# Performance work log

Measured on AMD Instinct MI355X. Metric: run time of the kernel, lower is better.

## Reference

```python
import jax, jax.numpy as jnp
import numpy as np

HEAD = 64            # RWKV_HEAD_SIZE
C = 1024             # n_embd = dim_att
F = 4096             # dim_ffn
B, T = 8, 256
H = C // HEAD
N_LAYER, LAYER_ID = 12, 1
GN_EPS = 1e-5 * 8 ** 2   # GroupNorm eps = 1e-5 * head_size_divisor^2


def bshift(x):
    """bidirectional_shift_multihead: per head, first half of channels shifted
    forward in time (right), second half shifted backward (left), zero-padded."""
    b, t, c = x.shape
    x4 = x.reshape(b, t, c // HEAD, HEAD)
    mid = HEAD // 2
    f = jnp.pad(x4[:, :-1, :, :mid], ((0, 0), (1, 0), (0, 0), (0, 0)))
    r = jnp.pad(x4[:, 1:, :, mid:], ((0, 0), (0, 1), (0, 0), (0, 0)))
    return jnp.concatenate([f, r], -1).reshape(b, t, c)


def layernorm(x, g, b):
    m = jnp.mean(x, -1, keepdims=True)
    v = jnp.mean((x - m) ** 2, -1, keepdims=True)
    return (x - m) * jax.lax.rsqrt(v + 1e-5) * g + b


def groupnorm(x, g, b):
    bb, t, c = x.shape
    xg = x.reshape(bb, t, H, HEAD)
    m = jnp.mean(xg, -1, keepdims=True)
    v = jnp.mean((xg - m) ** 2, -1, keepdims=True)
    return ((xg - m) * jax.lax.rsqrt(v + GN_EPS)).reshape(bb, t, c) * g + b


def wkv6_bi(r, k, v, w, u):
    """Bidirectional WKV6. r,k,v,w: [B,T,H,N]; u: [H,N].
    y_t = r_t . (S^fwd_t + u*k_t v_t^T + S^bwd_t), with per-channel decay
    d_t = exp(-exp(w_t)) applied to the state after each step in each direction."""
    d = jnp.exp(-jnp.exp(w))
    rT, kT, vT, dT = (jnp.moveaxis(a, 1, 0) for a in (r, k, v, d))  # [T,B,H,N]
    S0 = jnp.zeros((B, H, HEAD, HEAD), r.dtype)
    uB = u[None]  # [1,H,N]

    def fstep(S, inp):
        rt, kt, vt, dt = inp
        kv = kt[..., None] * vt[..., None, :]              # [B,H,N,N]
        y = jnp.einsum('bhj,bhji->bhi', rt, S + uB[..., None] * kv)
        return dt[..., None] * S + kv, y

    _, yf = jax.lax.scan(fstep, S0, (rT, kT, vT, dT))

    def bstep(S, inp):
        rt, kt, vt, dt = inp
        y = jnp.einsum('bhj,bhji->bhi', rt, S)
        return dt[..., None] * S + kt[..., None] * vt[..., None, :], y

    _, yb = jax.lax.scan(bstep, S0, (rT, kT, vT, dT), reverse=True)
    return jnp.moveaxis(yf + yb, 0, 1)  # [B,T,H,N]


def block_forward(x, ln1_g, ln1_b, ln2_g, ln2_b,
                  maa_x, maa_w, maa_k, maa_v, maa_r, maa_g, maa_w1, maa_w2,
                  time_decay, tdw1, tdw2, u, Wr, Wk, Wv, Wg, Wo, lnx_g, lnx_b,
                  cmaa_k, cmaa_r, Wck, Wcv, Wcr):
    # ---- RWKV_Tmix_V6 (attention) branch ----
    xa = layernorm(x, ln1_g, ln1_b)
    xx = bshift(xa) - xa
    a = jnp.tanh((xa + xx * maa_x) @ maa_w1).reshape(B, T, 5, -1)   # [B,T,5,32]
    m = jnp.einsum('btfd,fdc->fbtc', a, maa_w2)                      # [5,B,T,C]
    xw = xa + xx * (maa_w + m[0])
    xk = xa + xx * (maa_k + m[1])
    xv = xa + xx * (maa_v + m[2])
    xr = xa + xx * (maa_r + m[3])
    xg = xa + xx * (maa_g + m[4])
    r = (xr @ Wr).reshape(B, T, H, HEAD)
    k = (xk @ Wk).reshape(B, T, H, HEAD)
    v = (xv @ Wv).reshape(B, T, H, HEAD)
    g = jax.nn.silu(xg @ Wg)
    w = (time_decay + jnp.tanh(xw @ tdw1) @ tdw2).reshape(B, T, H, HEAD)
    y = wkv6_bi(r, k, v, w, u).reshape(B, T, C)
    y = groupnorm(y, lnx_g, lnx_b)
    x = x + (y * g) @ Wo
    # ---- RWKV_CMix_V6 (FFN) branch ----
    xc = layernorm(x, ln2_g, ln2_b)
    cxx = bshift(xc) - xc
    kk = jnp.square(jax.nn.relu((xc + cxx * cmaa_k) @ Wck))
    kv = kk @ Wcv
    x = x + jax.nn.sigmoid((xc + cxx * cmaa_r) @ Wcr) * kv
    return x


def setup_inputs() -> dict:
    key = jax.random.key(0)
    ks = jax.random.split(key, 16)
    r1 = 1.0 - LAYER_ID / N_LAYER            # ratio_1_to_almost0
    r0 = LAYER_ID / (N_LAYER - 1)            # ratio_0_to_1
    ddd = np.arange(C, dtype=np.float64) / C
    base = (1.0 - ddd ** r1).astype(np.float32)
    half = (1.0 - ddd ** (0.5 * r1)).astype(np.float32)
    s = 0.02
    p = {}
    p['x'] = jax.random.normal(ks[0], (B, T, C), jnp.float32)
    p['ln1_g'] = jnp.ones((C,), jnp.float32)
    p['ln1_b'] = jnp.zeros((C,), jnp.float32)
    p['ln2_g'] = jnp.ones((C,), jnp.float32)
    p['ln2_b'] = jnp.zeros((C,), jnp.float32)
    p['maa_x'] = jnp.asarray(base)
    p['maa_w'] = jnp.asarray(base)
    p['maa_k'] = jnp.asarray(base)
    p['maa_v'] = jnp.asarray((1.0 - (ddd ** r1 + 0.3 * r0)).astype(np.float32))
    p['maa_r'] = jnp.asarray(half)
    p['maa_g'] = jnp.asarray(half)
    p['maa_w1'] = jax.random.uniform(ks[1], (C, 160), jnp.float32, -0.01, 0.01)
    p['maa_w2'] = jax.random.uniform(ks[2], (5, 32, C), jnp.float32, -0.01, 0.01)
    n = np.arange(C, dtype=np.float64)
    p['time_decay'] = jnp.asarray((-6.0 + 5.0 * (n / (C - 1)) ** (0.7 + 1.3 * r0)).astype(np.float32))
    p['tdw1'] = jax.random.uniform(ks[3], (C, 64), jnp.float32, -0.01, 0.01)
    p['tdw2'] = jax.random.uniform(ks[4], (64, C), jnp.float32, -0.01, 0.01)
    faaaa = r0 * (1.0 - n / (C - 1)) + ((n + 1) % 3 - 1) * 0.1
    p['u'] = jnp.asarray(faaaa.reshape(H, HEAD).astype(np.float32))
    p['Wr'] = jax.random.normal(ks[5], (C, C), jnp.float32) * s
    p['Wk'] = jax.random.normal(ks[6], (C, C), jnp.float32) * s
    p['Wv'] = jax.random.normal(ks[7], (C, C), jnp.float32) * s
    p['Wg'] = jax.random.normal(ks[8], (C, C), jnp.float32) * s
    p['Wo'] = jax.random.normal(ks[9], (C, C), jnp.float32) * s
    p['lnx_g'] = jnp.ones((C,), jnp.float32)
    p['lnx_b'] = jnp.zeros((C,), jnp.float32)
    p['cmaa_k'] = jnp.asarray(base)
    p['cmaa_r'] = jnp.asarray(base)
    p['Wck'] = jax.random.normal(ks[10], (C, F), jnp.float32) * s
    p['Wcv'] = jax.random.normal(ks[11], (F, C), jnp.float32) * s
    p['Wcr'] = jax.random.normal(ks[12], (C, C), jnp.float32) * s
    return p


def reference(x, ln1_g, ln1_b, ln2_g, ln2_b,
              maa_x, maa_w, maa_k, maa_v, maa_r, maa_g, maa_w1, maa_w2,
              time_decay, tdw1, tdw2, u, Wr, Wk, Wv, Wg, Wo, lnx_g, lnx_b,
              cmaa_k, cmaa_r, Wck, Wcv, Wcr):
    return block_forward(x, ln1_g, ln1_b, ln2_g, ln2_b,
                         maa_x, maa_w, maa_k, maa_v, maa_r, maa_g, maa_w1, maa_w2,
                         time_decay, tdw1, tdw2, u, Wr, Wk, Wv, Wg, Wo, lnx_g, lnx_b,
                         cmaa_k, cmaa_r, Wck, Wcv, Wcr)
```

## Files before the change

### kernel.cpp

```cpp
#include <hip/hip_runtime.h>
#include <math.h>
#include <stdint.h>

static constexpr int B  = 8;
static constexpr int T  = 256;
static constexpr int C  = 1024;
static constexpr int H  = 16;
static constexpr int HEAD = 64;
static constexpr int FF = 4096;
static constexpr int BT = B * T;
static constexpr int NCH = 8;
static constexpr int CS  = 32;

typedef short short8  __attribute__((ext_vector_type(8)));
typedef float floatx4 __attribute__((ext_vector_type(4)));

__device__ __forceinline__ float bf2f(ushort u) {
    return __uint_as_float(((uint32_t)u) << 16);
}
__device__ __forceinline__ ushort f2bf(float x) {
    uint32_t u = __float_as_uint(x);
    u += 0x7fff + ((u >> 16) & 1);
    return (ushort)(u >> 16);
}

__device__ __forceinline__ void gload16(const void* g, void* l) {
    __builtin_amdgcn_global_load_lds(
        (const __attribute__((address_space(1))) unsigned int*)g,
        (__attribute__((address_space(3))) unsigned int*)l, 16, 0, 0);
}

#define BEPI_NONE_BF   0
#define BEPI_SILU_BF   1
#define BEPI_RELUSQ_BF 2
#define BEPI_NONE_F    3
#define BEPI_RES_F     4
#define BEPI_SIGRES_F  5
#define BEPI_TANH_F    6
#define BEPI_TANH_BF   7
#define BEPI_DECAY_F   8
#define BEPI_SIGRES2_F 9

__device__ __forceinline__ void red6(float (&vals)[6], float* red)
{
    const int wave = threadIdx.x >> 6, lane = threadIdx.x & 63;
#pragma unroll
    for (int i = 0; i < 6; ++i) {
        float v = vals[i];
#pragma unroll
        for (int off = 32; off > 0; off >>= 1) v += __shfl_xor(v, off);
        if (lane == 0) red[i * 4 + wave] = v;
    }
    __syncthreads();
#pragma unroll
    for (int i = 0; i < 6; ++i)
        vals[i] = red[i * 4 + 0] + red[i * 4 + 1] + red[i * 4 + 2] + red[i * 4 + 3];
}

__global__ __launch_bounds__(256) void lnshiftmix_kernel(const float* __restrict__ x,
                                                         const float* __restrict__ g,
                                                         const float* __restrict__ b,
                                                         const float* __restrict__ maa,
                                                         float* __restrict__ xa,
                                                         float* __restrict__ xx,
                                                         ushort* __restrict__ ax)
{
    const int row = blockIdx.x;
    const int t = row & (T - 1);
    const int tid = threadIdx.x;
    __shared__ float red[24];
    const float4 vc = reinterpret_cast<const float4*>(x + (size_t)row * C)[tid];
    float4 vp = make_float4(0.f, 0.f, 0.f, 0.f), vn = make_float4(0.f, 0.f, 0.f, 0.f);
    if (t > 0)     vp = reinterpret_cast<const float4*>(x + (size_t)(row - 1) * C)[tid];
    if (t < T - 1) vn = reinterpret_cast<const float4*>(x + (size_t)(row + 1) * C)[tid];
    float vals[6];
    vals[0] = vc.x + vc.y + vc.z + vc.w;
    vals[1] = vc.x * vc.x + vc.y * vc.y + vc.z * vc.z + vc.w * vc.w;
    vals[2] = vp.x + vp.y + vp.z + vp.w;
    vals[3] = vp.x * vp.x + vp.y * vp.y + vp.z * vp.z + vp.w * vp.w;
    vals[4] = vn.x + vn.y + vn.z + vn.w;
    vals[5] = vn.x * vn.x + vn.y * vn.y + vn.z * vn.z + vn.w * vn.w;
    red6(vals, red);
    const float mc = vals[0] * (1.f / C);
    const float rc = rsqrtf(fmaxf(vals[1] * (1.f / C) - mc * mc, 0.f) + 1e-5f);
    const float mp = vals[2] * (1.f / C);
    const float rp = rsqrtf(fmaxf(vals[3] * (1.f / C) - mp * mp, 0.f) + 1e-5f);
    const float mn = vals[4] * (1.f / C);
    const float rn = rsqrtf(fmaxf(vals[5] * (1.f / C) - mn * mn, 0.f) + 1e-5f);

    const int c = tid * 4;
    const bool fh = ((c & 63) < 32);
    const float cur[4] = {vc.x, vc.y, vc.z, vc.w};
    const float nbr[4] = {fh ? vp.x : vn.x, fh ? vp.y : vn.y,
                          fh ? vp.z : vn.z, fh ? vp.w : vn.w};
    const float mN = fh ? mp : mn, rN = fh ? rp : rn;
    const bool nvalid = fh ? (t > 0) : (t < T - 1);
    const size_t rb = (size_t)row * C;
#pragma unroll
    for (int e = 0; e < 4; ++e) {
        const float gg = g[c + e], bb = b[c + e];
        const float av = (cur[e] - mc) * rc * gg + bb;
        const float sv = nvalid ? ((nbr[e] - mN) * rN * gg + bb) : 0.f;
        const float xv = sv - av;
        xa[rb + c + e] = av;
        xx[rb + c + e] = xv;
        ax[rb + c + e] = f2bf(av + xv * maa[c + e]);
    }
}

__global__ __launch_bounds__(256) void lnshiftcmix_kernel(const float* __restrict__ x,
                                                          const float* __restrict__ g,
                                                          const float* __restrict__ b,
                                                          const float* __restrict__ mk,
                                                          const float* __restrict__ mr,
                                                          ushort* __restrict__ ok,
                                                          ushort* __restrict__ orr)
{
    const int row = blockIdx.x;
    const int t = row & (T - 1);
    const int tid = threadIdx.x;
    __shared__ float red[24];
    const float4 vc = reinterpret_cast<const float4*>(x + (size_t)row * C)[tid];
    float4 vp = make_float4(0.f, 0.f, 0.f, 0.f), vn = make_float4(0.f, 0.f, 0.f, 0.f);
    if (t > 0)     vp = reinterpret_cast<const float4*>(x + (size_t)(row - 1) * C)[tid];
    if (t < T - 1) vn = reinterpret_cast<const float4*>(x + (size_t)(row + 1) * C)[tid];
    float vals[6];
    vals[0] = vc.x + vc.y + vc.z + vc.w;
    vals[1] = vc.x * vc.x + vc.y * vc.y + vc.z * vc.z + vc.w * vc.w;
    vals[2] = vp.x + vp.y + vp.z + vp.w;
    vals[3] = vp.x * vp.x + vp.y * vp.y + vp.z * vp.z + vp.w * vp.w;
    vals[4] = vn.x + vn.y + vn.z + vn.w;
    vals[5] = vn.x * vn.x + vn.y * vn.y + vn.z * vn.z + vn.w * vn.w;
    red6(vals, red);
    const float mc = vals[0] * (1.f / C);
    const float rc = rsqrtf(fmaxf(vals[1] * (1.f / C) - mc * mc, 0.f) + 1e-5f);
    const float mp = vals[2] * (1.f / C);
    const float rp = rsqrtf(fmaxf(vals[3] * (1.f / C) - mp * mp, 0.f) + 1e-5f);
    const float mn = vals[4] * (1.f / C);
    const float rn = rsqrtf(fmaxf(vals[5] * (1.f / C) - mn * mn, 0.f) + 1e-5f);

    const int c = tid * 4;
    const bool fh = ((c & 63) < 32);
    const float cur[4] = {vc.x, vc.y, vc.z, vc.w};
    const float nbr[4] = {fh ? vp.x : vn.x, fh ? vp.y : vn.y,
                          fh ? vp.z : vn.z, fh ? vp.w : vn.w};
    const float mN = fh ? mp : mn, rN = fh ? rp : rn;
    const bool nvalid = fh ? (t > 0) : (t < T - 1);
    const size_t rb = (size_t)row * C;
#pragma unroll
    for (int e = 0; e < 4; ++e) {
        const float gg = g[c + e], bb = b[c + e];
        const float av = (cur[e] - mc) * rc * gg + bb;
        const float sv = nvalid ? ((nbr[e] - mN) * rN * gg + bb) : 0.f;
        const float xv = sv - av;
        ok[rb + c + e]  = f2bf(av + xv * mk[c + e]);
        orr[rb + c + e] = f2bf(av + xv * mr[c + e]);
    }
}

__global__ __launch_bounds__(1024) void gnmul_kernel(const ushort* __restrict__ yf,
                                                     const ushort* __restrict__ yb,
                                                     const float* __restrict__ g,
                                                     const float* __restrict__ b,
                                                     const ushort* __restrict__ gate,
                                                     const ushort* __restrict__ vin,
                                                     const ushort* __restrict__ rbuf,
                                                     const ushort* __restrict__ kbuf,
                                                     const float* __restrict__ u,
                                                     ushort* __restrict__ out)
{
    const int row = blockIdx.x;
    const int tid = threadIdx.x;
    const size_t idx = (size_t)row * C + tid;
    float p = bf2f(rbuf[idx]) * bf2f(kbuf[idx]) * u[tid];
#pragma unroll
    for (int off = 32; off > 0; off >>= 1) p += __shfl_xor(p, off);
    const float v = bf2f(yf[idx]) + bf2f(yb[idx]) + p * bf2f(vin[idx]);
    float s = v;
#pragma unroll
    for (int off = 32; off > 0; off >>= 1) s += __shfl_xor(s, off);
    const float m = s * (1.0f / HEAD);
    const float d = v - m;
    float q = d * d;
#pragma unroll
    for (int off = 32; off > 0; off >>= 1) q += __shfl_xor(q, off);
    const float rstd = rsqrtf(q * (1.0f / HEAD) + 6.4e-4f);
    out[idx] = f2bf((d * rstd * g[tid] + b[tid]) * bf2f(gate[idx]));
}

__global__ __launch_bounds__(256) void wconv_kernel(const float* __restrict__ W,
                                                    ushort* __restrict__ Wt,
                                                    int Kd, int Nd)
{
    __shared__ float tile[32][33];
    const int n0 = blockIdx.x * 32, k0 = blockIdx.y * 32;
    const int tx = threadIdx.x, ty = threadIdx.y;
#pragma unroll
    for (int i = 0; i < 4; ++i)
        tile[ty * 4 + i][tx] = W[(size_t)(k0 + ty * 4 + i) * Nd + n0 + tx];
    __syncthreads();
#pragma unroll
    for (int i = 0; i < 4; ++i)
        Wt[(size_t)(n0 + ty * 4 + i) * Kd + k0 + tx] = f2bf(tile[tx][ty * 4 + i]);
}

__global__ __launch_bounds__(256) void w2conv_kernel(const float* __restrict__ w2,
                                                     ushort* __restrict__ w2t)
{
    __shared__ float tile[32][33];
    const int f = blockIdx.y;
    const int n0 = blockIdx.x * 32;
    const int tx = threadIdx.x, ty = threadIdx.y;
#pragma unroll
    for (int i = 0; i < 4; ++i)
        tile[ty * 4 + i][tx] = w2[(size_t)f * 32 * C + (size_t)(ty * 4 + i) * C + n0 + tx];
    __syncthreads();
#pragma unroll
    for (int i = 0; i < 4; ++i)
        w2t[(size_t)f * C * 32 + (size_t)(n0 + ty * 4 + i) * 32 + tx] = f2bf(tile[tx][ty * 4 + i]);
}

struct Wconv4Args { const float* W[4]; };
__global__ __launch_bounds__(256) void wconv4_kernel(Wconv4Args args, ushort* __restrict__ Wt)
{
    __shared__ float tile[32][33];
    const int z = blockIdx.z;
    const float* __restrict__ W = args.W[z];
    ushort* __restrict__ dst = Wt + (size_t)z * C * C;
    const int n0 = blockIdx.x * 32, k0 = blockIdx.y * 32;
    const int tx = threadIdx.x, ty = threadIdx.y;
#pragma unroll
    for (int i = 0; i < 4; ++i)
        tile[ty * 4 + i][tx] = W[(size_t)(k0 + ty * 4 + i) * C + n0 + tx];
    __syncthreads();
#pragma unroll
    for (int i = 0; i < 4; ++i)
        dst[(size_t)(n0 + ty * 4 + i) * C + k0 + tx] = f2bf(tile[tx][ty * 4 + i]);
}

struct Mix5Args { const float* maa[5]; ushort* out[5]; };
__global__ __launch_bounds__(256) void mix5m_kernel(const ushort* __restrict__ a5b,
                                                    const ushort* __restrict__ w2t,
                                                    const float* __restrict__ xa,
                                                    const float* __restrict__ xx,
                                                    Mix5Args args)
{
    __shared__ __align__(16) ushort As[128 * 32];
    __shared__ __align__(16) ushort Bs[64 * 32];
    const int f = blockIdx.z;
    const int bm = blockIdx.y * 128, bn = blockIdx.x * 64;
    const int tid = threadIdx.x;
    const int wid = tid >> 6, lane = tid & 63;
    const int wr = wid >> 1, wc = wid & 1;
    const int l15 = lane & 15, lhi = lane >> 4;

#pragma unroll
    for (int p = 0; p < 2; ++p) {
        const int lin = p * 256 + tid;
        const int row = lin >> 2;
        const int sp = (lin & 3) ^ ((row >> 1) & 3);
        gload16(a5b + (size_t)(bm + row) * 160 + f * 32 + sp * 8, &As[lin * 8]);
    }
    {
        const int lin = tid;
        const int n = lin >> 2;
        const int sp = (lin & 3) ^ ((n >> 1) & 3);
        gload16(w2t + ((size_t)f * C + bn + n) * 32 + sp * 8, &Bs[lin * 8]);
    }
    __syncthreads();

    short8 af[4], bfr[2];
#pragma unroll
    for (int m = 0; m < 4; ++m) {
        const int row = wr * 64 + m * 16 + l15;
        const int sp = lhi ^ ((row >> 1) & 3);
        af[m] = *(const short8*)&As[row * 32 + sp * 8];
    }
#pragma unroll
    for (int n = 0; n < 2; ++n) {
        const int col = wc * 32 + n * 16 + l15;
        const int sp = lhi ^ ((col >> 1) & 3);
        bfr[n] = *(const short8*)&Bs[col * 32 + sp * 8];
    }
    floatx4 acc[4][2];
#pragma unroll
    for (int m = 0; m < 4; ++m)
#pragma unroll
        for (int n = 0; n < 2; ++n)
            acc[m][n] = __builtin_amdgcn_mfma_f32_16x16x32_bf16(
                af[m], bfr[n], (floatx4){0.f, 0.f, 0.f, 0.f}, 0, 0, 0);

    const float* __restrict__ maa = args.maa[f];
    ushort* __restrict__ out = args.out[f];
#pragma unroll
    for (int m = 0; m < 4; ++m) {
        const int row0 = bm + wr * 64 + m * 16 + lhi * 4;
#pragma unroll
        for (int n = 0; n < 2; ++n) {
            const int col = bn + wc * 32 + n * 16 + l15;
            const float mc = maa[col];
#pragma unroll
            for (int j = 0; j < 4; ++j) {
                const size_t oi = (size_t)(row0 + j) * C + col;
                out[oi] = f2bf(xa[oi] + xx[oi] * (mc + acc[m][n][j]));
            }
        }
    }
}

__global__ __launch_bounds__(256) void wkv_pass1(const ushort* __restrict__ k,
                                                 const ushort* __restrict__ v,
                                                 const float* __restrict__ d,
                                                 ushort* __restrict__ M,
                                                 float* __restrict__ D)
{
    const int uc = blockIdx.x;
    const int c = uc & (NCH - 1), unit = uc >> 3;
    const int dir = unit & 1, bh = unit >> 1;
    const int tid = threadIdx.x;
    const int wv = tid >> 6, lane = tid & 63;
    const int l15 = lane & 15, lhi = lane >> 4;
    const size_t rowb = ((size_t)(bh >> 4) * T * H + (bh & 15)) * HEAD;
    const int s0 = c * CS;

    __shared__ ushort kT[64][40];
    __shared__ ushort vt[64][40];
    __shared__ float  Ldd[CS][64];

    for (int idx = tid; idx < CS * 64; idx += 256) {
        const int s = idx >> 6, j = idx & 63;
        const int t = dir ? (T - 1 - (s0 + s)) : (s0 + s);
        const size_t g = rowb + (size_t)t * (H * HEAD) + j;
        kT[j][s] = k[g];
        vt[j][s] = v[g];
        Ldd[s][j] = d[g];
    }
    __syncthreads();

    if (tid < 64) {
        const int j = tid;
        float G = 1.f;
#pragma unroll
        for (int s = CS - 1; s >= 0; --s) {
            kT[j][s] = f2bf(bf2f(kT[j][s]) * G);
            G *= Ldd[s][j];
        }
        D[(size_t)uc * 64 + j] = G;
    }
    __syncthreads();

    const short8 av = *(const short8*)&vt[wv * 16 + l15][lhi * 8];
    ushort* __restrict__ mrow = M + (size_t)uc * 4096;
#pragma unroll
    for (int n = 0; n < 4; ++n) {
        const short8 bk = *(const short8*)&kT[n * 16 + l15][lhi * 8];
        const floatx4 acc = __builtin_amdgcn_mfma_f32_16x16x32_bf16(
            av, bk, (floatx4){0.f, 0.f, 0.f, 0.f}, 0, 0, 0);
#pragma unroll
        for (int jr = 0; jr < 4; ++jr) {
            const int i = wv * 16 + lhi * 4 + jr;
            mrow[(size_t)i * 64 + n * 16 + l15] = f2bf(acc[jr]);
        }
    }
}

__global__ __launch_bounds__(1024) void wkv_pass2(ushort* __restrict__ M,
                                                  const float* __restrict__ D)
{
    const int unit = blockIdx.x;
    const int tid = threadIdx.x;
    const int j0 = (tid & 15) * 4;
    float S0 = 0.f, S1 = 0.f, S2 = 0.f, S3 = 0.f;
#pragma unroll
    for (int c = 0; c < NCH; ++c) {
        const int uc = unit * NCH + c;
        const float4 Dv = *reinterpret_cast<const float4*>(D + (size_t)uc * 64 + j0);
        ushort* mp = M + (size_t)uc * 4096 + tid * 4;
        const uint2 mv = *reinterpret_cast<const uint2*>(mp);
        const float m0 = bf2f((ushort)(mv.x & 0xffff));
        const float m1 = bf2f((ushort)(mv.x >> 16));
        const float m2 = bf2f((ushort)(mv.y & 0xffff));
        const float m3 = bf2f((ushort)(mv.y >> 16));
        uint2 sv;
        sv.x = (uint32_t)f2bf(S0) | ((uint32_t)f2bf(S1) << 16);
        sv.y = (uint32_t)f2bf(S2) | ((uint32_t)f2bf(S3) << 16);
        *reinterpret_cast<uint2*>(mp) = sv;
        S0 = fmaf(Dv.x, S0, m0);
        S1 = fmaf(Dv.y, S1, m1);
        S2 = fmaf(Dv.z, S2, m2);
        S3 = fmaf(Dv.w, S3, m3);
    }
}

__global__ __launch_bounds__(256) void wkv_ymfma(const ushort* __restrict__ r,
                                                 const ushort* __restrict__ k,
                                                 const ushort* __restrict__ v,
                                                 const float* __restrict__ d,
                                                 const ushort* __restrict__ Sin,
                                                 ushort* __restrict__ yf,
                                                 ushort* __restrict__ yb)
{
    const int uc = blockIdx.x;
    const int c = uc & (NCH - 1), unit = uc >> 3;
    const int dir = unit & 1, bh = unit >> 1;
    const int tid = threadIdx.x;
    const int wv = tid >> 6, lane = tid & 63;
    const int l15 = lane & 15, lhi = lane >> 4;
    const size_t rowb = ((size_t)(bh >> 4) * T * H + (bh & 15)) * HEAD;
    const int s0 = c * CS;

    __shared__ ushort rp[32][64];
    __shared__ ushort kp[32][64];
    __shared__ ushort vt[64][40];
    __shared__ ushort Pl[32][32];
    __shared__ float  Ldd[CS][64];

    for (int idx = tid; idx < 32 * 64; idx += 256) {
        const int s = idx >> 6, j = idx & 63;
        const int t = dir ? (T - 1 - (s0 + s)) : (s0 + s);
        const size_t g = rowb + (size_t)t * (H * HEAD) + j;
        const int cs = (j >> 3) ^ (s & 7);
        rp[s][cs * 8 + (j & 7)] = r[g];
        kp[s][cs * 8 + (j & 7)] = k[g];
        vt[j][s] = v[g];
        Ldd[s][j] = d[g];
    }
    __syncthreads();

    if (wv == 0) {
        const int j = lane;
        float Q = 1.f;
#pragma unroll
        for (int s = 0; s < 32; ++s) {
            const int a = ((j >> 3) ^ (s & 7)) * 8 + (j & 7);
            rp[s][a] = f2bf(bf2f(rp[s][a]) * Q);
            Q *= Ldd[s][j];
        }
    } else if (wv == 1) {
        const int j = lane;
        float iQ = 1.f;
#pragma unroll
        for (int s = 0; s < 32; ++s) {
            iQ *= (1.0f / Ldd[s][j]);
            const int a = ((j >> 3) ^ (s & 7)) * 8 + (j & 7);
            kp[s][a] = f2bf(bf2f(kp[s][a]) * iQ);
        }
    }
    __syncthreads();

    const int st = wv & 1;
    const int ip = wv >> 1;

    short8 ar[2];
#pragma unroll
    for (int ks = 0; ks < 2; ++ks) {
        const int row = st * 16 + l15;
        const int ch = (ks * 4 + lhi) ^ (row & 7);
        ar[ks] = *(const short8*)&rp[row][ch * 8];
    }

    floatx4 acc[2];
#pragma unroll
    for (int n = 0; n < 2; ++n) {
        const int i = ip * 32 + n * 16 + l15;
        const ushort* sp = Sin + (size_t)uc * 4096 + (size_t)i * 64;
        const short8 b0 = *(const short8*)&sp[lhi * 8];
        const short8 b1 = *(const short8*)&sp[32 + lhi * 8];
        acc[n] = __builtin_amdgcn_mfma_f32_16x16x32_bf16(ar[0], b0, (floatx4){0.f, 0.f, 0.f, 0.f}, 0, 0, 0);
        acc[n] = __builtin_amdgcn_mfma_f32_16x16x32_bf16(ar[1], b1, acc[n], 0, 0, 0);
    }

    if (wv < 2) {
#pragma unroll
        for (int ut = 0; ut < 2; ++ut) {
            const int urow = ut * 16 + l15;
            const short8 bk0 = *(const short8*)&kp[urow][((0 + lhi) ^ (urow & 7)) * 8];
            const short8 bk1 = *(const short8*)&kp[urow][((4 + lhi) ^ (urow & 7)) * 8];
            floatx4 pa = __builtin_amdgcn_mfma_f32_16x16x32_bf16(ar[0], bk0, (floatx4){0.f, 0.f, 0.f, 0.f}, 0, 0, 0);
            pa = __builtin_amdgcn_mfma_f32_16x16x32_bf16(ar[1], bk1, pa, 0, 0, 0);
            const int sg0 = st * 16 + lhi * 4;
            const int ug = ut * 16 + l15;
#pragma unroll
            for (int jr = 0; jr < 4; ++jr) {
                const float val = (ug < sg0 + jr) ? pa[jr] : 0.f;
                Pl[sg0 + jr][ug] = f2bf(val);
            }
        }
    }
    __syncthreads();

    short8 ap;
    {
        const int row = st * 16 + l15;
        ap = *(const short8*)&Pl[row][lhi * 8];
    }
#pragma unroll
    for (int n = 0; n < 2; ++n) {
        const int i = ip * 32 + n * 16 + l15;
        const short8 bv = *(const short8*)&vt[i][lhi * 8];
        acc[n] = __builtin_amdgcn_mfma_f32_16x16x32_bf16(ap, bv, acc[n], 0, 0, 0);
    }

    ushort* __restrict__ yo = dir ? yb : yf;
#pragma unroll
    for (int n = 0; n < 2; ++n) {
        const int i = ip * 32 + n * 16 + l15;
#pragma unroll
        for (int jr = 0; jr < 4; ++jr) {
            const int sg = st * 16 + lhi * 4 + jr;
            const int t = dir ? (T - 1 - (s0 + sg)) : (s0 + sg);
            yo[rowb + (size_t)t * (H * HEAD) + i] = f2bf(acc[n][jr]);
        }
    }
}

template <int BN>
struct GemmLds {
    ushort As[2][128 * 64];
    ushort Bs[2][BN * 64];
};

template <int BN>
__device__ __forceinline__ void gemm_body(const ushort* __restrict__ A,
                                          const ushort* __restrict__ Bt,
                                          int bm, int bn, int K, int lda, int ldb,
                                          GemmLds<BN>& lds,
                                          floatx4 (&acc)[4][BN / 32])
{
    constexpr int NF = BN / 32;
    const int tid = threadIdx.x;
    const int wid = tid >> 6, lane = tid & 63;
    const int wr = wid >> 1, wc = wid & 1;
    const int l15 = lane & 15, lhi = lane >> 4;
    const int NT = K >> 6;

    auto stage = [&](int buf, int k0) {
#pragma unroll
        for (int p = 0; p < 4; ++p) {
            const int lin = p * 256 + tid;
            const int row = lin >> 3;
            const int cs = (lin & 7) ^ (row & 7);
            gload16(A + (size_t)(bm + row) * lda + k0 + cs * 8, &lds.As[buf][lin * 8]);
        }
#pragma unroll
        for (int p = 0; p < NF; ++p) {
            const int lin = p * 256 + tid;
            const int n = lin >> 3;
            const int cs = (lin & 7) ^ (n & 7);
            gload16(Bt + (size_t)(bn + n) * ldb + k0 + cs * 8, &lds.Bs[buf][lin * 8]);
        }
    };

    stage(0, 0);
    __syncthreads();
    for (int t = 0; t < NT; ++t) {
        const int cur = t & 1;
        if (t + 1 < NT) stage(cur ^ 1, (t + 1) << 6);

        short8 af[4][2];
#pragma unroll
        for (int m = 0; m < 4; ++m) {
            const int row = wr * 64 + m * 16 + l15;
#pragma unroll
            for (int s = 0; s < 2; ++s) {
                const int cc = (s * 4 + lhi) ^ (row & 7);
                af[m][s] = *(const short8*)&lds.As[cur][row * 64 + cc * 8];
            }
        }
        short8 bf[NF][2];
#pragma unroll
        for (int n = 0; n < NF; ++n) {
            const int col = wc * (BN / 2) + n * 16 + l15;
#pragma unroll
            for (int s = 0; s < 2; ++s) {
                const int cc = (s * 4 + lhi) ^ (col & 7);
                bf[n][s] = *(const short8*)&lds.Bs[cur][col * 64 + cc * 8];
            }
        }
#pragma unroll
        for (int m = 0; m < 4; ++m)
#pragma unroll
            for (int n = 0; n < NF; ++n) {
                acc[m][n] = __builtin_amdgcn_mfma_f32_16x16x32_bf16(af[m][0], bf[n][0], acc[m][n], 0, 0, 0);
                acc[m][n] = __builtin_amdgcn_mfma_f32_16x16x32_bf16(af[m][1], bf[n][1], acc[m][n], 0, 0, 0);
            }
        __syncthreads();
    }
}

template <int BN, int EPI>
__global__ __launch_bounds__(256) void bgemm_kernel(const ushort* __restrict__ A,
                                                    const ushort* __restrict__ Bt,
                                                    void* __restrict__ Cm,
                                                    int M, int N, int K,
                                                    const float* __restrict__ aux1,
                                                    const float* __restrict__ aux2,
                                                    const float* __restrict__ aux3)
{
    constexpr int NF = BN / 32;
    __shared__ GemmLds<BN> lds;
    int w = blockIdx.y * gridDim.x + blockIdx.x;
    const int nwg = gridDim.x * gridDim.y;
    if ((nwg & 7) == 0) w = (w & 7) * (nwg >> 3) + (w >> 3);
    const int bn = (w % gridDim.x) * BN;
    const int bm = (w / gridDim.x) * 128;
    const int tid = threadIdx.x;
    const int wid = tid >> 6, lane = tid & 63;
    const int wr = wid >> 1, wc = wid & 1;
    const int l15 = lane & 15, lhi = lane >> 4;

    floatx4 acc[4][NF];
#pragma unroll
    for (int m = 0; m < 4; ++m)
#pragma unroll
        for (int n = 0; n < NF; ++n) acc[m][n] = (floatx4){0.f, 0.f, 0.f, 0.f};

    gemm_body<BN>(A, Bt, bm, bn, K, K, K, lds, acc);

#pragma unroll
    for (int m = 0; m < 4; ++m) {
        const int row0 = bm + wr * 64 + m * 16 + lhi * 4;
#pragma unroll
        for (int n = 0; n < NF; ++n) {
            const int col = bn + wc * (BN / 2) + n * 16 + l15;
            if (col >= N) continue;
#pragma unroll
            for (int j = 0; j < 4; ++j) {
                const size_t oi = (size_t)(row0 + j) * N + col;
                const float a = acc[m][n][j];
                if constexpr (EPI == BEPI_NONE_BF) {
                    ((ushort*)Cm)[oi] = f2bf(a);
                } else if constexpr (EPI == BEPI_SILU_BF) {
                    ((ushort*)Cm)[oi] = f2bf(a / (1.f + __expf(-a)));
                } else if constexpr (EPI == BEPI_RELUSQ_BF) {
                    const float t = fmaxf(a, 0.f);
                    ((ushort*)Cm)[oi] = f2bf(t * t);
                } else if constexpr (EPI == BEPI_NONE_F) {
                    ((float*)Cm)[oi] = a;
                } else if constexpr (EPI == BEPI_RES_F) {
                    ((float*)Cm)[oi] = aux1[oi] + a;
                } else if constexpr (EPI == BEPI_SIGRES_F) {
                    ((float*)Cm)[oi] = aux1[oi] + aux2[oi] / (1.f + __expf(-a));
                } else if constexpr (EPI == BEPI_SIGRES2_F) {
                    const float kv = bf2f(((const ushort*)aux2)[oi]) +
                                     bf2f(((const ushort*)aux3)[oi]);
                    ((float*)Cm)[oi] = aux1[oi] + kv / (1.f + __expf(-a));
                } else if constexpr (EPI == BEPI_TANH_F) {
                    ((float*)Cm)[oi] = tanhf(a);
                } else if constexpr (EPI == BEPI_TANH_BF) {
                    ((ushort*)Cm)[oi] = f2bf(tanhf(a));
                } else {
                    ((float*)Cm)[oi] = __expf(-__expf(a + aux1[col]));
                }
            }
        }
    }
}

__global__ __launch_bounds__(256) void wcv_kernel(const ushort* __restrict__ A,
                                                  const ushort* __restrict__ Bt,
                                                  ushort* __restrict__ P0,
                                                  ushort* __restrict__ P1)
{
    __shared__ GemmLds<64> lds;
    const int z = blockIdx.z;
    int w = blockIdx.y * gridDim.x + blockIdx.x;
    w = (w & 7) * 32 + (w >> 3);
    const int bn = (w % 16) * 64;
    const int bm = (w / 16) * 128;
    const int tid = threadIdx.x;
    const int wid = tid >> 6, lane = tid & 63;
    const int wr = wid >> 1, wc = wid & 1;
    const int l15 = lane & 15, lhi = lane >> 4;

    floatx4 acc[4][2];
#pragma unroll
    for (int m = 0; m < 4; ++m)
#pragma unroll
        for (int n = 0; n < 2; ++n) acc[m][n] = (floatx4){0.f, 0.f, 0.f, 0.f};

    gemm_body<64>(A + z * (FF / 2), Bt + z * (FF / 2), bm, bn, FF / 2, FF, FF, lds, acc);

    ushort* __restrict__ P = z ? P1 : P0;
#pragma unroll
    for (int m = 0; m < 4; ++m) {
        const int row0 = bm + wr * 64 + m * 16 + lhi * 4;
#pragma unroll
        for (int n = 0; n < 2; ++n) {
            const int col = bn + wc * 32 + n * 16 + l15;
#pragma unroll
            for (int j = 0; j < 4; ++j)
                P[(size_t)(row0 + j) * C + col] = f2bf(acc[m][n][j]);
        }
    }
}

struct QkvgArgs { const ushort* A[4]; ushort* O[4]; };
__global__ __launch_bounds__(256) void qkvg_kernel(QkvgArgs args,
                                                   const ushort* __restrict__ Wt)
{
    __shared__ GemmLds<128> lds;
    const int z = blockIdx.z;
    int w = blockIdx.y * gridDim.x + blockIdx.x;
    w = (w & 7) * 16 + (w >> 3);
    const int bn = (w & 7) * 128;
    const int bm = (w >> 3) * 128;
    const int tid = threadIdx.x;
    const int wid = tid >> 6, lane = tid & 63;
    const int wr = wid >> 1, wc = wid & 1;
    const int l15 = lane & 15, lhi = lane >> 4;

    floatx4 acc[4][4];
#pragma unroll
    for (int m = 0; m < 4; ++m)
#pragma unroll
        for (int n = 0; n < 4; ++n) acc[m][n] = (floatx4){0.f, 0.f, 0.f, 0.f};

    gemm_body<128>(args.A[z], Wt + (size_t)z * C * C, bm, bn, C, C, C, lds, acc);

    ushort* __restrict__ O = args.O[z];
    const bool silu = (z == 3);
#pragma unroll
    for (int m = 0; m < 4; ++m) {
        const int row0 = bm + wr * 64 + m * 16 + lhi * 4;
#pragma unroll
        for (int n = 0; n < 4; ++n) {
            const int col = bn + wc * 64 + n * 16 + l15;
#pragma unroll
            for (int j = 0; j < 4; ++j) {
                float a = acc[m][n][j];
                if (silu) a = a / (1.f + __expf(-a));
                O[(size_t)(row0 + j) * C + col] = f2bf(a);
            }
        }
    }
}

extern "C" void kernel_launch(void* const* d_in, const int* in_sizes, int n_in,
                              void* d_out, int out_size, void* d_ws, size_t ws_size,
                              hipStream_t stream)
{
    const float* x        = (const float*)d_in[0];
    const float* ln1_g    = (const float*)d_in[1];
    const float* ln1_b    = (const float*)d_in[2];
    const float* ln2_g    = (const float*)d_in[3];
    const float* ln2_b    = (const float*)d_in[4];
    const float* maa_x    = (const float*)d_in[5];
    const float* maa_w    = (const float*)d_in[6];
    const float* maa_k    = (const float*)d_in[7];
    const float* maa_v    = (const float*)d_in[8];
    const float* maa_r    = (const float*)d_in[9];
    const float* maa_g    = (const float*)d_in[10];
    const float* maa_w1   = (const float*)d_in[11];
    const float* maa_w2   = (const float*)d_in[12];
    const float* time_dec = (const float*)d_in[13];
    const float* tdw1     = (const float*)d_in[14];
    const float* tdw2     = (const float*)d_in[15];
    const float* u        = (const float*)d_in[16];
    const float* Wr       = (const float*)d_in[17];
    const float* Wk       = (const float*)d_in[18];
    const float* Wv       = (const float*)d_in[19];
    const float* Wg       = (const float*)d_in[20];
    const float* Wo       = (const float*)d_in[21];
    const float* lnx_g    = (const float*)d_in[22];
    const float* lnx_b    = (const float*)d_in[23];
    const float* cmaa_k   = (const float*)d_in[24];
    const float* cmaa_r   = (const float*)d_in[25];
    const float* Wck      = (const float*)d_in[26];
    const float* Wcv      = (const float*)d_in[27];
    const float* Wcr      = (const float*)d_in[28];
    float* out = (float*)d_out;

    float* fws = (float*)d_ws;
    const size_t E = (size_t)BT * C;
    float* xa  = fws + 0 * E;
    float* xx  = fws + 1 * E;
    float* wd  = fws + 2 * E;
    float* fs  = fws + 3 * E;
    ushort* wBuf = (ushort*)(fws + 4 * E);
    ushort* Mbuf = (ushort*)fs;
    ushort* w2t  = wBuf + (size_t)C * 160;
    ushort* bf1  = wBuf + (size_t)C * FF;
    ushort* rb   = bf1 + E;
    ushort* kb   = rb + E;
    ushort* vb   = kb + E;
    ushort* gb   = vb + E;
    ushort* t1b  = gb + E;
    float* a5    = (float*)(t1b + (size_t)BT * 64);
    float* sig   = a5 + (size_t)BT * 160;
    float* Dbuf  = sig + (size_t)BT * H;
    ushort* a5b  = (ushort*)a5;
    ushort* xvb  = (ushort*)fs;
    ushort* xrb  = (ushort*)fs + E;
    ushort* xgb  = (ushort*)out;
    ushort* xwb  = (ushort*)out + E;
    ushort* yfb  = (ushort*)xa;
    ushort* ybb  = (ushort*)xa + E;
    ushort* p0b  = (ushort*)fs;
    ushort* p1b  = (ushort*)fs + E;
    ushort* kk   = (ushort*)xa;

    const dim3 blk(256);
    const dim3 tblk(32, 8);
    const dim3 gNN(C / 64, BT / 128);

    lnshiftmix_kernel<<<BT, blk, 0, stream>>>(x, ln1_g, ln1_b, maa_x, xa, xx, bf1);
    wconv_kernel<<<dim3(160 / 32, C / 32), tblk, 0, stream>>>(maa_w1, wBuf, C, 160);
    bgemm_kernel<64, BEPI_TANH_BF><<<dim3(3, BT / 128), blk, 0, stream>>>(bf1, wBuf, a5b, BT, 160, C, nullptr, nullptr, nullptr);

    w2conv_kernel<<<dim3(C / 32, 5), tblk, 0, stream>>>(maa_w2, w2t);

    Mix5Args margs;
    margs.maa[0] = maa_w; margs.maa[1] = maa_k; margs.maa[2] = maa_v;
    margs.maa[3] = maa_r; margs.maa[4] = maa_g;
    margs.out[0] = xwb; margs.out[1] = bf1; margs.out[2] = xvb;
    margs.out[3] = xrb; margs.out[4] = xgb;
    mix5m_kernel<<<dim3(C / 64, BT / 128, 5), blk, 0, stream>>>(a5b, w2t, xa, xx, margs);

    wconv_kernel<<<dim3(64 / 32, C / 32), tblk, 0, stream>>>(tdw1, wBuf, C, 64);
    bgemm_kernel<64, BEPI_TANH_BF><<<dim3(1, BT / 128), blk, 0, stream>>>(xwb, wBuf, t1b, BT, 64, C, nullptr, nullptr, nullptr);
    wconv_kernel<<<dim3(C / 32, 64 / 32), tblk, 0, stream>>>(tdw2, wBuf, 64, C);
    bgemm_kernel<64, BEPI_DECAY_F><<<gNN, blk, 0, stream>>>(t1b, wBuf, wd, BT, C, 64, time_dec, nullptr, nullptr);

    Wconv4Args wargs;
    wargs.W[0] = Wk; wargs.W[1] = Wv; wargs.W[2] = Wr; wargs.W[3] = Wg;
    wconv4_kernel<<<dim3(C / 32, C / 32, 4), tblk, 0, stream>>>(wargs, wBuf);
    QkvgArgs qargs;
    qargs.A[0] = bf1; qargs.A[1] = xvb; qargs.A[2] = xrb; qargs.A[3] = xgb;
    qargs.O[0] = kb;  qargs.O[1] = vb;  qargs.O[2] = rb;  qargs.O[3] = gb;
    qkvg_kernel<<<dim3(8, 16, 4), blk, 0, stream>>>(qargs, wBuf);

    wkv_pass1<<<dim3(2 * B * H * NCH), blk, 0, stream>>>(kb, vb, wd, Mbuf, Dbuf);
    wkv_pass2<<<dim3(2 * B * H), dim3(1024), 0, stream>>>(Mbuf, Dbuf);
    wkv_ymfma<<<dim3(2 * B * H * NCH), blk, 0, stream>>>(rb, kb, vb, wd, Mbuf, yfb, ybb);

    gnmul_kernel<<<BT, dim3(1024), 0, stream>>>(yfb, ybb, lnx_g, lnx_b, gb, vb, rb, kb, u, vb);
    wconv_kernel<<<dim3(C / 32, C / 32), tblk, 0, stream>>>(Wo, wBuf, C, C);
    bgemm_kernel<64, BEPI_RES_F><<<gNN, blk, 0, stream>>>(vb, wBuf, out, BT, C, C, x, nullptr, nullptr);

    lnshiftcmix_kernel<<<BT, blk, 0, stream>>>(out, ln2_g, ln2_b, cmaa_k, cmaa_r, bf1, gb);
    wconv_kernel<<<dim3(FF / 32, C / 32), tblk, 0, stream>>>(Wck, wBuf, C, FF);
    bgemm_kernel<128, BEPI_RELUSQ_BF><<<dim3(FF / 128, BT / 128), blk, 0, stream>>>(bf1, wBuf, kk, BT, FF, C, nullptr, nullptr, nullptr);
    wconv_kernel<<<dim3(C / 32, FF / 32), tblk, 0, stream>>>(Wcv, wBuf, FF, C);
    wcv_kernel<<<dim3(16, 16, 2), blk, 0, stream>>>(kk, wBuf, p0b, p1b);
    wconv_kernel<<<dim3(C / 32, C / 32), tblk, 0, stream>>>(Wcr, wBuf, C, C);
    bgemm_kernel<64, BEPI_SIGRES2_F><<<gNN, blk, 0, stream>>>(gb, wBuf, out, BT, C, C, out, (const float*)p0b, (const float*)p1b);

    (void)in_sizes; (void)n_in; (void)out_size; (void)ws_size;
}
```

Before: 251.3 us.

## Use 512-thread GEMM workgroups and batch weight conversions into fewer launches

All GEMM kernels now run with 8 waves per 512-thread workgroup. Each wave owns a narrower slice of columns, so it needs fewer accumulators while the LDS tile stays the same. Several small weight transpose/convert launches are merged into one multi-job kernel at the start, and the Wcv and Wcr conversions are merged into one launch. This cuts launch count and serialization. The Wcr weights go into a spare buffer (rb) so they can share that launch, and each wave now issues fewer MFMAs per LDS fragment load.

```diff
diff --git a/kernel.cpp b/kernel.cpp
--- a/kernel.cpp
+++ b/kernel.cpp
@@ -188,6 +188,36 @@
     out[idx] = f2bf((d * rstd * g[tid] + b[tid]) * bf2f(gate[idx]));
 }
 
+struct WJobs {
+    const float* W[8];
+    ushort* dst[8];
+    int Kd[8], Nd[8], ntx[8], base[8];
+    int njobs;
+};
+__global__ __launch_bounds__(256) void wconvB_kernel(WJobs jobs)
+{
+    __shared__ float tile[32][33];
+    const int bid = blockIdx.x;
+    int j = 0;
+#pragma unroll
+    for (int i = 1; i < 8; ++i)
+        if (i < jobs.njobs && bid >= jobs.base[i]) j = i;
+    const float* __restrict__ W = jobs.W[j];
+    ushort* __restrict__ dst = jobs.dst[j];
+    const int Kd = jobs.Kd[j], Nd = jobs.Nd[j];
+    const int local = bid - jobs.base[j];
+    const int n0 = (local % jobs.ntx[j]) * 32;
+    const int k0 = (local / jobs.ntx[j]) * 32;
+    const int tx = threadIdx.x, ty = threadIdx.y;
+#pragma unroll
+    for (int i = 0; i < 4; ++i)
+        tile[ty * 4 + i][tx] = W[(size_t)(k0 + ty * 4 + i) * Nd + n0 + tx];
+    __syncthreads();
+#pragma unroll
+    for (int i = 0; i < 4; ++i)
+        dst[(size_t)(n0 + ty * 4 + i) * Kd + k0 + tx] = f2bf(tile[tx][ty * 4 + i]);
+}
+
 __global__ __launch_bounds__(256) void wconv_kernel(const float* __restrict__ W,
                                                     ushort* __restrict__ Wt,
                                                     int Kd, int Nd)
@@ -202,22 +232,6 @@
 #pragma unroll
     for (int i = 0; i < 4; ++i)
         Wt[(size_t)(n0 + ty * 4 + i) * Kd + k0 + tx] = f2bf(tile[tx][ty * 4 + i]);
-}
-
-__global__ __launch_bounds__(256) void w2conv_kernel(const float* __restrict__ w2,
-                                                     ushort* __restrict__ w2t)
-{
-    __shared__ float tile[32][33];
-    const int f = blockIdx.y;
-    const int n0 = blockIdx.x * 32;
-    const int tx = threadIdx.x, ty = threadIdx.y;
-#pragma unroll
-    for (int i = 0; i < 4; ++i)
-        tile[ty * 4 + i][tx] = w2[(size_t)f * 32 * C + (size_t)(ty * 4 + i) * C + n0 + tx];
-    __syncthreads();
-#pragma unroll
-    for (int i = 0; i < 4; ++i)
-        w2t[(size_t)f * C * 32 + (size_t)(n0 + ty * 4 + i) * 32 + tx] = f2bf(tile[tx][ty * 4 + i]);
 }
 
 struct Wconv4Args { const float* W[4]; };
@@ -521,30 +535,30 @@
 };
 
 template <int BN>
-__device__ __forceinline__ void gemm_body(const ushort* __restrict__ A,
-                                          const ushort* __restrict__ Bt,
-                                          int bm, int bn, int K, int lda, int ldb,
-                                          GemmLds<BN>& lds,
-                                          floatx4 (&acc)[4][BN / 32])
-{
-    constexpr int NF = BN / 32;
+__device__ __forceinline__ void gemm_body8(const ushort* __restrict__ A,
+                                           const ushort* __restrict__ Bt,
+                                           int bm, int bn, int K, int lda, int ldb,
+                                           GemmLds<BN>& lds,
+                                           floatx4 (&acc)[4][BN / 64])
+{
+    constexpr int NF = BN / 64;
     const int tid = threadIdx.x;
     const int wid = tid >> 6, lane = tid & 63;
-    const int wr = wid >> 1, wc = wid & 1;
+    const int wr = wid >> 2, wc = wid & 3;
     const int l15 = lane & 15, lhi = lane >> 4;
     const int NT = K >> 6;
 
     auto stage = [&](int buf, int k0) {
 #pragma unroll
-        for (int p = 0; p < 4; ++p) {
-            const int lin = p * 256 + tid;
+        for (int p = 0; p < 2; ++p) {
+            const int lin = p * 512 + tid;
             const int row = lin >> 3;
             const int cs = (lin & 7) ^ (row & 7);
             gload16(A + (size_t)(bm + row) * lda + k0 + cs * 8, &lds.As[buf][lin * 8]);
         }
 #pragma unroll
         for (int p = 0; p < NF; ++p) {
-            const int lin = p * 256 + tid;
+            const int lin = p * 512 + tid;
             const int n = lin >> 3;
             const int cs = (lin & 7) ^ (n & 7);
             gload16(Bt + (size_t)(bn + n) * ldb + k0 + cs * 8, &lds.Bs[buf][lin * 8]);
@@ -570,7 +584,7 @@
         short8 bf[NF][2];
 #pragma unroll
         for (int n = 0; n < NF; ++n) {
-            const int col = wc * (BN / 2) + n * 16 + l15;
+            const int col = wc * (BN / 4) + n * 16 + l15;
 #pragma unroll
             for (int s = 0; s < 2; ++s) {
                 const int cc = (s * 4 + lhi) ^ (col & 7);
@@ -589,7 +603,7 @@
 }
 
 template <int BN, int EPI>
-__global__ __launch_bounds__(256) void bgemm_kernel(const ushort* __restrict__ A,
+__global__ __launch_bounds__(512) void bgemm_kernel(const ushort* __restrict__ A,
                                                     const ushort* __restrict__ Bt,
                                                     void* __restrict__ Cm,
                                                     int M, int N, int K,
@@ -597,7 +611,7 @@
                                                     const float* __restrict__ aux2,
                                                     const float* __restrict__ aux3)
 {
-    constexpr int NF = BN / 32;
+    constexpr int NF = BN / 64;
     __shared__ GemmLds<BN> lds;
     int w = blockIdx.y * gridDim.x + blockIdx.x;
     const int nwg = gridDim.x * gridDim.y;
@@ -606,7 +620,7 @@
     const int bm = (w / gridDim.x) * 128;
     const int tid = threadIdx.x;
     const int wid = tid >> 6, lane = tid & 63;
-    const int wr = wid >> 1, wc = wid & 1;
+    const int wr = wid >> 2, wc = wid & 3;
     const int l15 = lane & 15, lhi = lane >> 4;
 
     floatx4 acc[4][NF];
@@ -615,14 +629,14 @@
 #pragma unroll
         for (int n = 0; n < NF; ++n) acc[m][n] = (floatx4){0.f, 0.f, 0.f, 0.f};
 
-    gemm_body<BN>(A, Bt, bm, bn, K, K, K, lds, acc);
+    gemm_body8<BN>(A, Bt, bm, bn, K, K, K, lds, acc);
 
 #pragma unroll
     for (int m = 0; m < 4; ++m) {
         const int row0 = bm + wr * 64 + m * 16 + lhi * 4;
 #pragma unroll
         for (int n = 0; n < NF; ++n) {
-            const int col = bn + wc * (BN / 2) + n * 16 + l15;
+            const int col = bn + wc * (BN / 4) + n * 16 + l15;
             if (col >= N) continue;
 #pragma unroll
             for (int j = 0; j < 4; ++j) {
@@ -657,7 +671,7 @@
     }
 }
 
-__global__ __launch_bounds__(256) void wcv_kernel(const ushort* __restrict__ A,
+__global__ __launch_bounds__(512) void wcv_kernel(const ushort* __restrict__ A,
                                                   const ushort* __restrict__ Bt,
                                                   ushort* __restrict__ P0,
                                                   ushort* __restrict__ P1)
@@ -670,33 +684,28 @@
     const int bm = (w / 16) * 128;
     const int tid = threadIdx.x;
     const int wid = tid >> 6, lane = tid & 63;
-    const int wr = wid >> 1, wc = wid & 1;
+    const int wr = wid >> 2, wc = wid & 3;
     const int l15 = lane & 15, lhi = lane >> 4;
 
-    floatx4 acc[4][2];
-#pragma unroll
-    for (int m = 0; m < 4; ++m)
-#pragma unroll
-        for (int n = 0; n < 2; ++n) acc[m][n] = (floatx4){0.f, 0.f, 0.f, 0.f};
-
-    gemm_body<64>(A + z * (FF / 2), Bt + z * (FF / 2), bm, bn, FF / 2, FF, FF, lds, acc);
+    floatx4 acc[4][1];
+#pragma unroll
+    for (int m = 0; m < 4; ++m) acc[m][0] = (floatx4){0.f, 0.f, 0.f, 0.f};
+
+    gemm_body8<64>(A + z * (FF / 2), Bt + z * (FF / 2), bm, bn, FF / 2, FF, FF, lds, acc);
 
     ushort* __restrict__ P = z ? P1 : P0;
 #pragma unroll
     for (int m = 0; m < 4; ++m) {
         const int row0 = bm + wr * 64 + m * 16 + lhi * 4;
-#pragma unroll
-        for (int n = 0; n < 2; ++n) {
-            const int col = bn + wc * 32 + n * 16 + l15;
-#pragma unroll
-            for (int j = 0; j < 4; ++j)
-                P[(size_t)(row0 + j) * C + col] = f2bf(acc[m][n][j]);
-        }
+        const int col = bn + wc * 16 + l15;
+#pragma unroll
+        for (int j = 0; j < 4; ++j)
+            P[(size_t)(row0 + j) * C + col] = f2bf(acc[m][0][j]);
     }
 }
 
 struct QkvgArgs { const ushort* A[4]; ushort* O[4]; };
-__global__ __launch_bounds__(256) void qkvg_kernel(QkvgArgs args,
+__global__ __launch_bounds__(512) void qkvg_kernel(QkvgArgs args,
                                                    const ushort* __restrict__ Wt)
 {
     __shared__ GemmLds<128> lds;
@@ -707,16 +716,16 @@
     const int bm = (w >> 3) * 128;
     const int tid = threadIdx.x;
     const int wid = tid >> 6, lane = tid & 63;
-    const int wr = wid >> 1, wc = wid & 1;
+    const int wr = wid >> 2, wc = wid & 3;
     const int l15 = lane & 15, lhi = lane >> 4;
 
-    floatx4 acc[4][4];
+    floatx4 acc[4][2];
 #pragma unroll
     for (int m = 0; m < 4; ++m)
 #pragma unroll
-        for (int n = 0; n < 4; ++n) acc[m][n] = (floatx4){0.f, 0.f, 0.f, 0.f};
-
-    gemm_body<128>(args.A[z], Wt + (size_t)z * C * C, bm, bn, C, C, C, lds, acc);
+        for (int n = 0; n < 2; ++n) acc[m][n] = (floatx4){0.f, 0.f, 0.f, 0.f};
+
+    gemm_body8<128>(args.A[z], Wt + (size_t)z * C * C, bm, bn, C, C, C, lds, acc);
 
     ushort* __restrict__ O = args.O[z];
     const bool silu = (z == 3);
@@ -724,8 +733,8 @@
     for (int m = 0; m < 4; ++m) {
         const int row0 = bm + wr * 64 + m * 16 + lhi * 4;
 #pragma unroll
-        for (int n = 0; n < 4; ++n) {
-            const int col = bn + wc * 64 + n * 16 + l15;
+        for (int n = 0; n < 2; ++n) {
+            const int col = bn + wc * 32 + n * 16 + l15;
 #pragma unroll
             for (int j = 0; j < 4; ++j) {
                 float a = acc[m][n][j];
@@ -780,6 +789,8 @@
     ushort* wBuf = (ushort*)(fws + 4 * E);
     ushort* Mbuf = (ushort*)fs;
     ushort* w2t  = wBuf + (size_t)C * 160;
+    ushort* t1wt = wBuf + (size_t)C * 320;
+    ushort* t2wt = wBuf + (size_t)C * 384;
     ushort* bf1  = wBuf + (size_t)C * FF;
     ushort* rb   = bf1 + E;
     ushort* kb   = rb + E;
@@ -801,14 +812,25 @@
     ushort* kk   = (ushort*)xa;
 
     const dim3 blk(256);
+    const dim3 gblk(512);
     const dim3 tblk(32, 8);
     const dim3 gNN(C / 64, BT / 128);
 
+    WJobs ej;
+    ej.njobs = 8;
+    ej.W[0] = maa_w1; ej.dst[0] = wBuf; ej.Kd[0] = C; ej.Nd[0] = 160; ej.ntx[0] = 5; ej.base[0] = 0;
+    for (int f = 0; f < 5; ++f) {
+        ej.W[1 + f] = maa_w2 + (size_t)f * 32 * C;
+        ej.dst[1 + f] = w2t + (size_t)f * C * 32;
+        ej.Kd[1 + f] = 32; ej.Nd[1 + f] = C; ej.ntx[1 + f] = 32;
+        ej.base[1 + f] = 160 + f * 32;
+    }
+    ej.W[6] = tdw1; ej.dst[6] = t1wt; ej.Kd[6] = C; ej.Nd[6] = 64; ej.ntx[6] = 2; ej.base[6] = 320;
+    ej.W[7] = tdw2; ej.dst[7] = t2wt; ej.Kd[7] = 64; ej.Nd[7] = C; ej.ntx[7] = 32; ej.base[7] = 384;
+    wconvB_kernel<<<dim3(448), tblk, 0, stream>>>(ej);
+
     lnshiftmix_kernel<<<BT, blk, 0, stream>>>(x, ln1_g, ln1_b, maa_x, xa, xx, bf1);
-    wconv_kernel<<<dim3(160 / 32, C / 32), tblk, 0, stream>>>(maa_w1, wBuf, C, 160);
-    bgemm_kernel<64, BEPI_TANH_BF><<<dim3(3, BT / 128), blk, 0, stream>>>(bf1, wBuf, a5b, BT, 160, C, nullptr, nullptr, nullptr);
-
-    w2conv_kernel<<<dim3(C / 32, 5), tblk, 0, stream>>>(maa_w2, w2t);
+    bgemm_kernel<64, BEPI_TANH_BF><<<dim3(3, BT / 128), gblk, 0, stream>>>(bf1, wBuf, a5b, BT, 160, C, nullptr, nullptr, nullptr);
 
     Mix5Args margs;
     margs.maa[0] = maa_w; margs.maa[1] = maa_k; margs.maa[2] = maa_v;
@@ -817,10 +839,8 @@
     margs.out[3] = xrb; margs.out[4] = xgb;
     mix5m_kernel<<<dim3(C / 64, BT / 128, 5), blk, 0, stream>>>(a5b, w2t, xa, xx, margs);
 
-    wconv_kernel<<<dim3(64 / 32, C / 32), tblk, 0, stream>>>(tdw1, wBuf, C, 64);
-    bgemm_kernel<64, BEPI_TANH_BF><<<dim3(1, BT / 128), blk, 0, stream>>>(xwb, wBuf, t1b, BT, 64, C, nullptr, nullptr, nullptr);
-    wconv_kernel<<<dim3(C / 32, 64 / 32), tblk, 0, stream>>>(tdw2, wBuf, 64, C);
-    bgemm_kernel<64, BEPI_DECAY_F><<<gNN, blk, 0, stream>>>(t1b, wBuf, wd, BT, C, 64, time_dec, nullptr, nullptr);
+    bgemm_kernel<64, BEPI_TANH_BF><<<dim3(1, BT / 128), gblk, 0, stream>>>(xwb, t1wt, t1b, BT, 64, C, nullptr, nullptr, nullptr);
+    bgemm_kernel<64, BEPI_DECAY_F><<<gNN, gblk, 0, stream>>>(t1b, t2wt, wd, BT, C, 64, time_dec, nullptr, nullptr);
 
     Wconv4Args wargs;
     wargs.W[0] = Wk; wargs.W[1] = Wv; wargs.W[2] = Wr; wargs.W[3] = Wg;
@@ -828,7 +848,7 @@
     QkvgArgs qargs;
     qargs.A[0] = bf1; qargs.A[1] = xvb; qargs.A[2] = xrb; qargs.A[3] = xgb;
     qargs.O[0] = kb;  qargs.O[1] = vb;  qargs.O[2] = rb;  qargs.O[3] = gb;
-    qkvg_kernel<<<dim3(8, 16, 4), blk, 0, stream>>>(qargs, wBuf);
+    qkvg_kernel<<<dim3(8, 16, 4), gblk, 0, stream>>>(qargs, wBuf);
 
     wkv_pass1<<<dim3(2 * B * H * NCH), blk, 0, stream>>>(kb, vb, wd, Mbuf, Dbuf);
     wkv_pass2<<<dim3(2 * B * H), dim3(1024), 0, stream>>>(Mbuf, Dbuf);
@@ -836,15 +856,21 @@
 
     gnmul_kernel<<<BT, dim3(1024), 0, stream>>>(yfb, ybb, lnx_g, lnx_b, gb, vb, rb, kb, u, vb);
     wconv_kernel<<<dim3(C / 32, C / 32), tblk, 0, stream>>>(Wo, wBuf, C, C);
-    bgemm_kernel<64, BEPI_RES_F><<<gNN, blk, 0, stream>>>(vb, wBuf, out, BT, C, C, x, nullptr, nullptr);
+    bgemm_kernel<64, BEPI_RES_F><<<gNN, gblk, 0, stream>>>(vb, wBuf, out, BT, C, C, x, nullptr, nullptr);
 
     lnshiftcmix_kernel<<<BT, blk, 0, stream>>>(out, ln2_g, ln2_b, cmaa_k, cmaa_r, bf1, gb);
     wconv_kernel<<<dim3(FF / 32, C / 32), tblk, 0, stream>>>(Wck, wBuf, C, FF);
-    bgemm_kernel<128, BEPI_RELUSQ_BF><<<dim3(FF / 128, BT / 128), blk, 0, stream>>>(bf1, wBuf, kk, BT, FF, C, nullptr, nullptr, nullptr);
-    wconv_kernel<<<dim3(C / 32, FF / 32), tblk, 0, stream>>>(Wcv, wBuf, FF, C);
-    wcv_kernel<<<dim3(16, 16, 2), blk, 0, stream>>>(kk, wBuf, p0b, p1b);
-    wconv_kernel<<<dim3(C / 32, C / 32), tblk, 0, stream>>>(Wcr, wBuf, C, C);
-    bgemm_kernel<64, BEPI_SIGRES2_F><<<gNN, blk, 0, stream>>>(gb, wBuf, out, BT, C, C, out, (const float*)p0b, (const float*)p1b);
+    bgemm_kernel<128, BEPI_RELUSQ_BF><<<dim3(FF / 128, BT / 128), gblk, 0, stream>>>(bf1, wBuf, kk, BT, FF, C, nullptr, nullptr, nullptr);
+
+    WJobs fj;
+    fj.njobs = 2;
+    fj.W[0] = Wcv; fj.dst[0] = wBuf; fj.Kd[0] = FF; fj.Nd[0] = C; fj.ntx[0] = 32; fj.base[0] = 0;
+    fj.W[1] = Wcr; fj.dst[1] = rb;   fj.Kd[1] = C;  fj.Nd[1] = C; fj.ntx[1] = 32; fj.base[1] = 4096;
+    for (int i = 2; i < 8; ++i) { fj.W[i] = nullptr; fj.dst[i] = nullptr; fj.Kd[i] = 1; fj.Nd[i] = 1; fj.ntx[i] = 1; fj.base[i] = 1 << 30; }
+    wconvB_kernel<<<dim3(4096 + 1024), tblk, 0, stream>>>(fj);
+
+    wcv_kernel<<<dim3(16, 16, 2), gblk, 0, stream>>>(kk, wBuf, p0b, p1b);
+    bgemm_kernel<64, BEPI_SIGRES2_F><<<gNN, gblk, 0, stream>>>(gb, rb, out, BT, C, C, out, (const float*)p0b, (const float*)p1b);
 
     (void)in_sizes; (void)n_in; (void)out_size; (void)ws_size;
 }
```

Result: faster. 233.8 us (-7.0%).
